# Performance work log

Measured on AMD Instinct MI355X. Metric: run time of the kernel, lower is better.

## Reference

```python
import jax, jax.numpy as jnp
import numpy as np

B, T = 256, 50
N_ITEMS = 100000
EMB = 256      # embedding
KBD = 128      # KBembedding == MN_dims
HID = 256      # layers[0] == layers[-1]
OUT = 256      # out_dim
NF = 10        # MN_nfactors == n_r


def setup_inputs() -> dict:
    key = jax.random.key(0)
    ks = jax.random.split(key, 18)
    s = 0.05
    return {
        "X": jax.random.randint(ks[0], (B, T), 0, N_ITEMS),
        "E": jax.random.normal(ks[1], (N_ITEMS, EMB), jnp.float32) * s,
        "KBE": jax.random.normal(ks[2], (N_ITEMS, KBD), jnp.float32) * s,
        "r_matrix": jax.random.normal(ks[3], (NF, KBD), jnp.float32) * s,
        "W_ih": jax.random.normal(ks[4], (3 * HID, EMB), jnp.float32) * s,
        "W_hh": jax.random.normal(ks[5], (3 * HID, HID), jnp.float32) * s,
        "b_ih": jnp.zeros((3 * HID,), jnp.float32),
        "b_hh": jnp.zeros((3 * HID,), jnp.float32),
        "MNu_W": jax.random.normal(ks[6], (KBD, HID), jnp.float32) * s,
        "MNu_b": jnp.zeros((KBD,), jnp.float32),
        "MNu2_W": jax.random.normal(ks[7], (HID, KBD + HID), jnp.float32) * s,
        "MNu2_b": jnp.zeros((HID,), jnp.float32),
        "MNea_W": jax.random.normal(ks[8], (KBD, KBD), jnp.float32) * s,
        "MNea_b": jnp.zeros((KBD,), jnp.float32),
        "mlp1_W": jax.random.normal(ks[9], (OUT, HID), jnp.float32) * s,
        "mlp1_b": jnp.zeros((OUT,), jnp.float32),
        "mlp2_W": jax.random.normal(ks[10], (OUT, EMB + KBD), jnp.float32) * s,
        "mlp2_b": jnp.zeros((OUT,), jnp.float32),
    }


def _gru_cell(x, h, W_ih, W_hh, b_ih, b_hh):
    # PyTorch GRUCell: gates stacked [r, z, n] along dim 0 of weights
    gi = x @ W_ih.T + b_ih
    gh = h @ W_hh.T + b_hh
    ir, iz, inn = jnp.split(gi, 3, axis=-1)
    hr, hz, hn = jnp.split(gh, 3, axis=-1)
    r = jax.nn.sigmoid(ir + hr)
    z = jax.nn.sigmoid(iz + hz)
    n = jnp.tanh(inn + r * hn)
    return (1.0 - z) * n + z * h


def reference(X, E, KBE, r_matrix, W_ih, W_hh, b_ih, b_hh,
              MNu_W, MNu_b, MNu2_W, MNu2_b, MNea_W, MNea_b,
              mlp1_W, mlp1_b, mlp2_W, mlp2_b):
    Bv, Tv = X.shape
    Em = E.at[0].set(0.0)     # mask row 0 of E
    KBm = KBE.at[0].set(0.0)  # mask row 0 of KBE
    Sx = Em[X]                # (B, T, EMB)
    KBItem = KBm[X]           # (B, T, KBD)

    def step(carry, xs):
        h, MN, y_sum = carry
        x_t, kb_t = xs                      # (B, EMB), (B, KBD)
        h = _gru_cell(x_t, h, W_ih, W_hh, b_ih, b_hh)
        y = h                                # dropout p=0 -> identity
        # gated memory write
        EA = jnp.tanh(kb_t @ MNea_W.T + MNea_b)          # (B, KBD)
        EA = EA[:, None, :] + r_matrix                    # (B, NF, KBD)
        gate = jax.nn.sigmoid(jnp.sum(MN * EA, axis=-1, keepdims=True))  # (B, NF, 1)
        MN = MN * (1.0 - gate) + EA * gate
        # attention read
        U = jnp.tanh(y @ MNu_W.T + MNu_b)                 # (B, KBD)
        AW = jax.nn.softmax(U @ r_matrix.T, axis=1)       # (B, NF)
        AC = jnp.einsum('bfd,bf->bd', MN, AW)             # (B, KBD)
        Ut = jnp.tanh(jnp.concatenate([y, AC], axis=-1) @ MNu2_W.T + MNu2_b)  # (B, HID)
        y_out = jnp.tanh(Ut @ mlp1_W.T + mlp1_b)          # (B, OUT)
        return (h, MN, y_sum + y_out), None

    init = (jnp.zeros((Bv, HID), Sx.dtype),
            jnp.zeros((Bv, NF, KBD), Sx.dtype),
            jnp.zeros((Bv, OUT), Sx.dtype))
    xs = (jnp.swapaxes(Sx, 0, 1), jnp.swapaxes(KBItem, 0, 1))  # (T, B, *)
    (h, MN, y_sum), _ = jax.lax.scan(step, init, xs)
    y = y_sum / Tv

    MergeE = jnp.concatenate([E, KBE], axis=1).at[0].set(0.0)  # (N, EMB+KBD)
    Sy = jnp.tanh(MergeE @ mlp2_W.T + mlp2_b)                  # (N, OUT)
    scores = jax.nn.log_softmax(y @ Sy.T, axis=1)              # (B, N)
    return scores, y
```

## Files before the change

kernel.cpp:

```cpp
#include <hip/hip_runtime.h>

typedef _Float16 f16;
typedef _Float16 f16x2 __attribute__((ext_vector_type(2)));
typedef _Float16 f16x8 __attribute__((ext_vector_type(8)));
typedef float f32x4 __attribute__((ext_vector_type(4)));
typedef int i32x4 __attribute__((ext_vector_type(4)));

#define MFMA16(a,b,c) __builtin_amdgcn_mfma_f32_16x16x32_f16(a,b,c,0,0,0)

#define NITEMS 100000
#define NBLK4  1563

#define OFF_WIH   0u
#define OFF_WHH   393216u
#define OFF_MNU   786432u
#define OFF_MNU2  851968u
#define OFF_MNEA  1048576u
#define OFF_MLP1  1081344u
#define OFF_MLP2  1212416u
#define OFF_WHHD  1409024u
#define OFF_GI    1802240u
#define OFF_TV    21463040u
#define OFF_MN    24739840u
#define OFF_YALL  57507840u
#define OFF_SY    64061440u
#define OFF_Y16   115261440u
#define OFF_PMAX  115392512u
#define OFF_PSUM  117030912u
#define OFF_LSE   118669312u

__device__ __forceinline__ float sigm(float x) { return 1.f / (1.f + __expf(-x)); }
__device__ __forceinline__ float tanh_fast(float x) {
  return 1.f - 2.f / (1.f + __expf(2.f * x));
}
__device__ __forceinline__ float fdot2(f16x2 a, f16x2 b, float c) {
#if defined(__has_builtin)
#if __has_builtin(__builtin_amdgcn_fdot2)
  return __builtin_amdgcn_fdot2(a, b, c, false);
#else
  return fmaf((float)a[1], (float)b[1], fmaf((float)a[0], (float)b[0], c));
#endif
#else
  return fmaf((float)a[1], (float)b[1], fmaf((float)a[0], (float)b[0], c));
#endif
}

__global__ __launch_bounds__(256) void k_pack(
    const float* s0, const float* s1, const float* s2, const float* s3,
    const float* s4, const float* s5, const float* s6, f16* base)
{
  int fid = blockIdx.x * 256 + threadIdx.x;
  if (fid >= 88064) {
    int g = fid - 88064;
    const float* sp = s1 + (size_t)g * 8;
    f16* dst = (f16*)((char*)base + OFF_WHHD);
    f16x8 v;
    #pragma unroll
    for (int j = 0; j < 8; j++) v[j] = (f16)sp[j];
    *(f16x8*)(dst + (size_t)g * 8) = v;
    return;
  }
  const float* src; f16* dst; int K, f;
  if (fid < 24576)      { src = s0; dst = base;          K = 256; f = fid; }
  else if (fid < 49152) { src = s1; dst = base + 196608; K = 256; f = fid - 24576; }
  else if (fid < 53248) { src = s2; dst = base + 393216; K = 256; f = fid - 49152; }
  else if (fid < 65536) { src = s3; dst = base + 425984; K = 384; f = fid - 53248; }
  else if (fid < 67584) { src = s4; dst = base + 524288; K = 128; f = fid - 65536; }
  else if (fid < 75776) { src = s5; dst = base + 540672; K = 256; f = fid - 67584; }
  else                  { src = s6; dst = base + 606208; K = 384; f = fid - 75776; }
  int lane = f & 63, t2 = f >> 6, KS = K >> 5;
  int ks = t2 % KS, nt = t2 / KS;
  int row = nt * 16 + (lane & 15), col = ks * 32 + ((lane >> 4) << 3);
  const float* sp = src + (size_t)row * K + col;
  f16x8 v;
  #pragma unroll
  for (int j = 0; j < 8; j++) v[j] = (f16)sp[j];
  *(f16x8*)(dst + (size_t)f * 8) = v;
}

__global__ __launch_bounds__(512) void k_prep(
    const int* __restrict__ X, const float* __restrict__ E,
    const f16* __restrict__ Wih_p, const float* __restrict__ bih,
    const float* __restrict__ bhh, f16* __restrict__ gi,
    const float* __restrict__ KBE, const f16* __restrict__ Wea_p,
    const float* __restrict__ bea, f16* __restrict__ tv)
{
  __shared__ __align__(16) char smem[66048];
  f16 (*At)[264] = (f16(*)[264])smem;
  f16* Lg2 = (f16*)(smem + 16896);
  int tid = threadIdx.x;
  int w = tid >> 6, lane = tid & 63, lr = lane & 15, lg = lane >> 4;
  if (blockIdx.x < 400) {
    int r0g = blockIdx.x * 32;
    int t = r0g >> 8;
    {
      int r = tid >> 4, c = (tid & 15) * 16;
      int b = (r0g + r) & 255;
      int item = X[b * 50 + t];
      if (item == 0) {
        #pragma unroll
        for (int j = 0; j < 16; j++) At[r][c + j] = (f16)0.f;
      } else {
        const float4* sp = (const float4*)(E + (size_t)item * 256 + c);
        #pragma unroll
        for (int q = 0; q < 4; q++) {
          float4 v = sp[q];
          At[r][c + q*4 + 0] = (f16)v.x; At[r][c + q*4 + 1] = (f16)v.y;
          At[r][c + q*4 + 2] = (f16)v.z; At[r][c + q*4 + 3] = (f16)v.w;
        }
      }
    }
    __syncthreads();
    f32x4 acc[2][6] = {};
    for (int ks = 0; ks < 8; ks++) {
      f16x8 a0 = *(const f16x8*)(&At[lr][ks * 32 + lg * 8]);
      f16x8 a1 = *(const f16x8*)(&At[16 + lr][ks * 32 + lg * 8]);
      #pragma unroll
      for (int j = 0; j < 6; j++) {
        int nt = w * 6 + j;
        f16x8 bf = *(const f16x8*)(Wih_p + ((size_t)((nt * 8 + ks) * 64 + lane) << 3));
        acc[0][j] = MFMA16(a0, bf, acc[0][j]);
        acc[1][j] = MFMA16(a1, bf, acc[1][j]);
      }
    }
    #pragma unroll
    for (int j = 0; j < 6; j++) {
      int col = (w * 6 + j) * 16 + lr;
      float bias = bih[col] + (col < 512 ? bhh[col] : 0.f);
      #pragma unroll
      for (int mt = 0; mt < 2; mt++)
        #pragma unroll
        for (int rr = 0; rr < 4; rr++)
          Lg2[(mt * 16 + lg * 4 + rr) * 768 + col] = (f16)(acc[mt][j][rr] + bias);
    }
    __syncthreads();
    f16* dst = gi + (size_t)r0g * 768;
    #pragma unroll
    for (int q = 0; q < 6; q++) {
      int u = q * 512 + tid;
      *(f16x8*)(dst + u * 8) = *(const f16x8*)(Lg2 + u * 8);
    }
  } else {
    int r0 = (blockIdx.x - 400) * 32;
    int t = r0 >> 8;
    {
      int r = tid >> 4, c = (tid & 15) * 8;
      int b = (r0 + r) & 255;
      int item = X[b * 50 + t];
      if (item == 0) {
        #pragma unroll
        for (int j = 0; j < 8; j++) At[r][c + j] = (f16)0.f;
      } else {
        const float4* sp = (const float4*)(KBE + (size_t)item * 128 + c);
        #pragma unroll
        for (int q = 0; q < 2; q++) {
          float4 v = sp[q];
          At[r][c + q*4 + 0] = (f16)v.x; At[r][c + q*4 + 1] = (f16)v.y;
          At[r][c + q*4 + 2] = (f16)v.z; At[r][c + q*4 + 3] = (f16)v.w;
        }
      }
    }
    __syncthreads();
    f32x4 acc[2] = {};
    for (int ks = 0; ks < 4; ks++) {
      f16x8 a0 = *(const f16x8*)(&At[lr][ks * 32 + lg * 8]);
      f16x8 a1 = *(const f16x8*)(&At[16 + lr][ks * 32 + lg * 8]);
      f16x8 bf = *(const f16x8*)(Wea_p + ((size_t)((w * 4 + ks) * 64 + lane) << 3));
      acc[0] = MFMA16(a0, bf, acc[0]);
      acc[1] = MFMA16(a1, bf, acc[1]);
    }
    f16* tvs = Lg2;
    int col = w * 16 + lr;
    float bias = bea[col];
    #pragma unroll
    for (int mt = 0; mt < 2; mt++)
      #pragma unroll
      for (int rr = 0; rr < 4; rr++)
        tvs[(mt * 16 + lg * 4 + rr) * 128 + col] = (f16)tanh_fast(acc[mt][rr] + bias);
    __syncthreads();
    {
      int row = tid >> 4, c = (tid & 15) * 8;
      *(f16x8*)(tv + (size_t)(r0 + row) * 128 + c) = *(const f16x8*)(tvs + row * 128 + c);
    }
  }
}

__global__ __launch_bounds__(1024) void k_fused2(
    const f16* __restrict__ Whh_d, const float* __restrict__ bhh,
    const f16* __restrict__ gi, f16* __restrict__ y_all,
    const f16* __restrict__ tv, const float* __restrict__ Rm, f16* __restrict__ MN,
    const float* __restrict__ E, const float* __restrict__ KBE,
    const f16* __restrict__ mlp2_p, const float* __restrict__ mlp2b, f16* __restrict__ Sy)
{
  __shared__ __align__(16) char smem[25088];
  int tid = threadIdx.x, w = tid >> 6, l = tid & 63;
  if (blockIdx.x < 256) {
    f16* hbuf = (f16*)smem;
    float* ghbuf = (float*)(smem + 1024);
    int b = blockIdx.x;
    int chunk = l >> 4, cl = l & 15;
    i32x4 Wv[3][8];
    #pragma unroll
    for (int j = 0; j < 3; j++) {
      int col = w * 48 + j * 16 + cl;
      const f16* wp = Whh_d + (size_t)col * 256 + chunk * 64;
      #pragma unroll
      for (int m = 0; m < 8; m++)
        Wv[j][m] = *(const i32x4*)(wp + m * 8);
    }
    float hprev = 0.f, bN = 0.f;
    f16 gr = (f16)0.f, gz = (f16)0.f, gn = (f16)0.f;
    if (tid < 256) {
      hbuf[(tid >> 6) * 72 + (tid & 63)] = (f16)0.f;
      bN = bhh[512 + tid];
      const f16* g0 = gi + (size_t)b * 768 + tid;
      gr = g0[0]; gz = g0[256]; gn = g0[512];
    }
    __syncthreads();
    const f16* hb = hbuf + chunk * 72;
    for (int t = 0; t < 50; t++) {
      float s0 = 0.f, s1 = 0.f, s2 = 0.f;
      #pragma unroll
      for (int m = 0; m < 8; m++) {
        i32x4 hw = *(const i32x4*)(hb + m * 8);
        #pragma unroll
        for (int p = 0; p < 4; p++) {
          f16x2 hp = __builtin_bit_cast(f16x2, hw[p]);
          s0 = fdot2(hp, __builtin_bit_cast(f16x2, Wv[0][m][p]), s0);
          s1 = fdot2(hp, __builtin_bit_cast(f16x2, Wv[1][m][p]), s1);
          s2 = fdot2(hp, __builtin_bit_cast(f16x2, Wv[2][m][p]), s2);
        }
      }
      s0 += __shfl_xor(s0, 16); s0 += __shfl_xor(s0, 32);
      s1 += __shfl_xor(s1, 16); s1 += __shfl_xor(s1, 32);
      s2 += __shfl_xor(s2, 16); s2 += __shfl_xor(s2, 32);
      if (l < 16) {
        ghbuf[w * 48 + l]      = s0;
        ghbuf[w * 48 + 16 + l] = s1;
        ghbuf[w * 48 + 32 + l] = s2;
      }
      __syncthreads();
      if (tid < 256) {
        int c = tid;
        float rg = sigm((float)gr + ghbuf[c]);
        float zg = sigm((float)gz + ghbuf[256 + c]);
        float ng = tanh_fast((float)gn + rg * (ghbuf[512 + c] + bN));
        float hv = ng + zg * (hprev - ng);
        hprev = hv;
        hbuf[(c >> 6) * 72 + (c & 63)] = (f16)hv;
        y_all[((size_t)t * 256 + b) * 256 + c] = (f16)hv;
        if (t < 49) {
          const f16* gN = gi + ((size_t)(t + 1) * 256 + b) * 768 + c;
          gr = gN[0]; gz = gN[256]; gn = gN[512];
        }
      }
      __syncthreads();
    }
  } else if (blockIdx.x < 416) {
    int lane = l;
    int pair = (blockIdx.x - 256) * 16 + w;
    int b = pair / 10, f = pair - (pair / 10) * 10;
    float r0_ = Rm[f * 128 + lane], r1_ = Rm[f * 128 + 64 + lane];
    float mn0 = 0.f, mn1 = 0.f;
    float c0 = (float)tv[(size_t)b * 128 + lane];
    float c1 = (float)tv[(size_t)b * 128 + 64 + lane];
    for (int t = 0; t < 50; t++) {
      float ea0 = c0 + r0_;
      float ea1 = c1 + r1_;
      if (t < 49) {
        size_t nb = ((size_t)(t + 1) * 256 + b) * 128;
        c0 = (float)tv[nb + lane];
        c1 = (float)tv[nb + 64 + lane];
      }
      float p = mn0 * ea0 + mn1 * ea1;
      #pragma unroll
      for (int off = 32; off > 0; off >>= 1) p += __shfl_xor(p, off);
      float g = sigm(p);
      mn0 += (ea0 - mn0) * g;
      mn1 += (ea1 - mn1) * g;
      size_t mb = (((size_t)t * 256 + b) * 10 + f) * 128;
      MN[mb + lane] = (f16)mn0;
      MN[mb + 64 + lane] = (f16)mn1;
    }
  } else {
    f16* At = (f16*)smem;
    int lane = l, lr = lane & 15, lg = lane >> 4;
    int i0 = (blockIdx.x - 416) * 32;
    {
      int r = tid >> 5;
      int item = i0 + r;
      int c = (tid & 31) * 8;
      if (item == 0) {
        #pragma unroll
        for (int j = 0; j < 8; j++) At[r * 392 + c + j] = (f16)0.f;
      } else {
        const float4* sp = (const float4*)(E + (size_t)item * 256 + c);
        #pragma unroll
        for (int q = 0; q < 2; q++) {
          float4 v = sp[q];
          At[r * 392 + c + q*4 + 0] = (f16)v.x; At[r * 392 + c + q*4 + 1] = (f16)v.y;
          At[r * 392 + c + q*4 + 2] = (f16)v.z; At[r * 392 + c + q*4 + 3] = (f16)v.w;
        }
      }
      int c2 = (tid & 31) * 4;
      if (item == 0) {
        #pragma unroll
        for (int j = 0; j < 4; j++) At[r * 392 + 256 + c2 + j] = (f16)0.f;
      } else {
        float4 v = *(const float4*)(KBE + (size_t)item * 128 + c2);
        At[r * 392 + 256 + c2 + 0] = (f16)v.x; At[r * 392 + 256 + c2 + 1] = (f16)v.y;
        At[r * 392 + 256 + c2 + 2] = (f16)v.z; At[r * 392 + 256 + c2 + 3] = (f16)v.w;
      }
    }
    __syncthreads();
    int mt = w & 1, ntp = w >> 1;
    f32x4 acc[2] = {};
    for (int ks = 0; ks < 12; ks++) {
      f16x8 a = *(const f16x8*)(&At[(mt * 16 + lr) * 392 + ks * 32 + lg * 8]);
      #pragma unroll
      for (int j = 0; j < 2; j++) {
        int nt = ntp * 2 + j;
        f16x8 bf = *(const f16x8*)(mlp2_p + ((size_t)((nt * 12 + ks) * 64 + lane) << 3));
        acc[j] = MFMA16(a, bf, acc[j]);
      }
    }
    #pragma unroll
    for (int j = 0; j < 2; j++) {
      int col = (ntp * 2 + j) * 16 + lr;
      float bias = mlp2b[col];
      #pragma unroll
      for (int rr = 0; rr < 4; rr++) {
        int item = i0 + mt * 16 + lg * 4 + rr;
        Sy[(size_t)item * 256 + col] = (f16)tanh_fast(acc[j][rr] + bias);
      }
    }
  }
}

__global__ __launch_bounds__(512) void k_uacut(
    const f16* __restrict__ y_all, const f16* __restrict__ MNu_p,
    const float* __restrict__ MNub, const float* __restrict__ Rm,
    const f16* __restrict__ MN,
    const f16* __restrict__ MNu2_p, const float* __restrict__ MNu2b,
    const f16* __restrict__ mlp1_p, const float* __restrict__ mlp1b,
    float* __restrict__ ypart)
{
  __shared__ __align__(16) char smem[25088];
  int tid = threadIdx.x, w = tid >> 6, lane = tid & 63, lr = lane & 15, lg = lane >> 4;
  f16   (*Aty)[264] = (f16(*)[264])smem;
  float (*Uf)[136]  = (float(*)[136])(smem + 8448);
  f16   (*Utl)[264] = (f16(*)[264])(smem + 8448);
  float (*Lg)[10]   = (float(*)[10])(smem + 17152);
  float (*Aw)[10]   = (float(*)[10])(smem + 17792);
  f16   (*ACs)[136] = (f16(*)[136])(smem + 18432);
  int r0 = blockIdx.x * 16;
  {
    int r = tid >> 5, c = (tid & 31) * 8;
    f16x8 v = *(const f16x8*)(y_all + (size_t)(r0 + r) * 256 + c);
    *(f16x8*)(&Aty[r][c]) = v;
  }
  __syncthreads();
  {
    f32x4 acc = {};
    for (int ks = 0; ks < 8; ks++) {
      f16x8 a = *(const f16x8*)(&Aty[lr][ks * 32 + lg * 8]);
      f16x8 bf = *(const f16x8*)(MNu_p + ((size_t)((w * 8 + ks) * 64 + lane) << 3));
      acc = MFMA16(a, bf, acc);
    }
    int col = w * 16 + lr;
    float bias = MNub[col];
    #pragma unroll
    for (int rr = 0; rr < 4; rr++)
      Uf[lg * 4 + rr][col] = tanh_fast(acc[rr] + bias);
  }
  __syncthreads();
  if (tid < 160) {
    int row = tid / 10, f = tid - (tid / 10) * 10;
    float s = 0.f;
    for (int d = 0; d < 128; d++) s += Uf[row][d] * Rm[f * 128 + d];
    Lg[row][f] = s;
  }
  __syncthreads();
  if (tid < 16) {
    float m = -1e30f;
    #pragma unroll
    for (int f = 0; f < 10; f++) m = fmaxf(m, Lg[tid][f]);
    float e[10], s = 0.f;
    #pragma unroll
    for (int f = 0; f < 10; f++) { e[f] = __expf(Lg[tid][f] - m); s += e[f]; }
    float inv = 1.f / s;
    #pragma unroll
    for (int f = 0; f < 10; f++) Aw[tid][f] = e[f] * inv;
  }
  __syncthreads();
  if (tid < 256) {
    int row = tid >> 4, d0 = (tid & 15) * 8;
    float a[8] = {0,0,0,0,0,0,0,0};
    for (int f = 0; f < 10; f++) {
      float wgt = Aw[row][f];
      f16x8 mv = *(const f16x8*)(MN + (((size_t)(r0 + row)) * 10 + f) * 128 + d0);
      #pragma unroll
      for (int q = 0; q < 8; q++) a[q] += wgt * (float)mv[q];
    }
    f16x8 o;
    #pragma unroll
    for (int q = 0; q < 8; q++) o[q] = (f16)a[q];
    *(f16x8*)(&ACs[row][d0]) = o;
  }
  __syncthreads();
  {
    f32x4 acc[2] = {};
    for (int ks = 0; ks < 12; ks++) {
      f16x8 a = (ks < 8)
        ? *(const f16x8*)(&Aty[lr][ks * 32 + lg * 8])
        : *(const f16x8*)(&ACs[lr][(ks - 8) * 32 + lg * 8]);
      #pragma unroll
      for (int j = 0; j < 2; j++) {
        f16x8 bf = *(const f16x8*)(MNu2_p + ((size_t)(((w * 2 + j) * 12 + ks) * 64 + lane) << 3));
        acc[j] = MFMA16(a, bf, acc[j]);
      }
    }
    __syncthreads();
    #pragma unroll
    for (int j = 0; j < 2; j++) {
      int col = (w * 2 + j) * 16 + lr;
      float bias = MNu2b[col];
      #pragma unroll
      for (int rr = 0; rr < 4; rr++)
        Utl[lg * 4 + rr][col] = (f16)tanh_fast(acc[j][rr] + bias);
    }
  }
  __syncthreads();
  {
    f32x4 acc2[2] = {};
    for (int ks = 0; ks < 8; ks++) {
      f16x8 a = *(const f16x8*)(&Utl[lr][ks * 32 + lg * 8]);
      #pragma unroll
      for (int j = 0; j < 2; j++) {
        f16x8 bf = *(const f16x8*)(mlp1_p + ((size_t)(((w * 2 + j) * 8 + ks) * 64 + lane) << 3));
        acc2[j] = MFMA16(a, bf, acc2[j]);
      }
    }
    #pragma unroll
    for (int j = 0; j < 2; j++) {
      int col = (w * 2 + j) * 16 + lr;
      float bias = mlp1b[col];
      #pragma unroll
      for (int rr = 0; rr < 4; rr++) {
        int row = r0 + lg * 4 + rr;
        ypart[(size_t)row * 256 + col] = tanh_fast(acc2[j][rr] + bias);
      }
    }
  }
}

__global__ __launch_bounds__(256) void k_yfin(
    const float* __restrict__ ypart, float* __restrict__ outy, f16* __restrict__ y16)
{
  int b = blockIdx.x, c = threadIdx.x;
  float s = 0.f;
  for (int t = 0; t < 50; t++) s += ypart[((size_t)t * 256 + b) * 256 + c];
  float v = s * (1.0f / 50.0f);
  outy[b * 256 + c] = v;
  y16[b * 256 + c] = (f16)v;
}

__global__ __launch_bounds__(512) void k_score0(
    const f16* __restrict__ y16, const f16* __restrict__ Sy,
    float* __restrict__ pmax, float* __restrict__ psum)
{
  __shared__ float pm[512], ps[512];
  int tid = threadIdx.x, w = tid >> 6, lane = tid & 63, lr = lane & 15, lg = lane >> 4;
  int i0 = blockIdx.x * 64;
  int mtb = (w >> 1) * 4, ntb = (w & 1) * 2;
  f32x4 acc[4][2] = {};
  for (int ks = 0; ks < 8; ks++) {
    f16x8 a[4];
    #pragma unroll
    for (int i = 0; i < 4; i++)
      a[i] = *(const f16x8*)(y16 + ((size_t)((mtb + i) * 16 + lr)) * 256 + ks * 32 + lg * 8);
    #pragma unroll
    for (int j = 0; j < 2; j++) {
      int item = i0 + (ntb + j) * 16 + lr;
      int ic = item < NITEMS ? item : (NITEMS - 1);
      f16x8 bv = *(const f16x8*)(Sy + (size_t)ic * 256 + ks * 32 + lg * 8);
      #pragma unroll
      for (int i = 0; i < 4; i++) acc[i][j] = MFMA16(a[i], bv, acc[i][j]);
    }
  }
  {
    int item0 = i0 + ntb * 16 + lr, item1 = item0 + 16;
    bool v0 = item0 < NITEMS, v1 = item1 < NITEMS;
    #pragma unroll
    for (int i = 0; i < 4; i++)
      #pragma unroll
      for (int rr = 0; rr < 4; rr++) {
        float x0 = v0 ? acc[i][0][rr] : -1e30f;
        float x1 = v1 ? acc[i][1][rr] : -1e30f;
        float m = fmaxf(x0, x1);
        m = fmaxf(m, __shfl_xor(m, 1)); m = fmaxf(m, __shfl_xor(m, 2));
        m = fmaxf(m, __shfl_xor(m, 4)); m = fmaxf(m, __shfl_xor(m, 8));
        float s = (v0 ? __expf(x0 - m) : 0.f) + (v1 ? __expf(x1 - m) : 0.f);
        s += __shfl_xor(s, 1); s += __shfl_xor(s, 2);
        s += __shfl_xor(s, 4); s += __shfl_xor(s, 8);
        if (lr == 0) {
          int row = (mtb + i) * 16 + lg * 4 + rr;
          pm[(w & 1) * 256 + row] = m;
          ps[(w & 1) * 256 + row] = s;
        }
      }
  }
  __syncthreads();
  if (tid < 256) {
    float m0 = pm[tid], m1 = pm[256 + tid];
    float s0 = ps[tid], s1 = ps[256 + tid];
    float M = fmaxf(m0, m1);
    float S = s0 * __expf(m0 - M) + s1 * __expf(m1 - M);
    pmax[(size_t)tid * 1600 + blockIdx.x] = M;
    psum[(size_t)tid * 1600 + blockIdx.x] = S;
  }
}

__global__ __launch_bounds__(256) void k_lse(
    const float* __restrict__ pmax, const float* __restrict__ psum, float* __restrict__ lse)
{
  int b = blockIdx.x, tid = threadIdx.x;
  __shared__ float red[256];
  float m = -1e30f;
  for (int i = tid; i < NBLK4; i += 256) m = fmaxf(m, pmax[(size_t)b * 1600 + i]);
  red[tid] = m; __syncthreads();
  for (int s = 128; s > 0; s >>= 1) {
    if (tid < s) red[tid] = fmaxf(red[tid], red[tid + s]);
    __syncthreads();
  }
  float M = red[0]; __syncthreads();
  float s = 0.f;
  for (int i = tid; i < NBLK4; i += 256)
    s += psum[(size_t)b * 1600 + i] * __expf(pmax[(size_t)b * 1600 + i] - M);
  red[tid] = s; __syncthreads();
  for (int q = 128; q > 0; q >>= 1) {
    if (tid < q) red[tid] += red[tid + q];
    __syncthreads();
  }
  if (tid == 0) lse[b] = M + logf(red[0]);
}

__global__ __launch_bounds__(512) void k_scores1(
    const f16* __restrict__ y16, const f16* __restrict__ Sy,
    const float* __restrict__ lse, float* __restrict__ out)
{
  __shared__ float lse_s[256];
  int tid = threadIdx.x, w = tid >> 6, lane = tid & 63, lr = lane & 15, lg = lane >> 4;
  if (tid < 256) lse_s[tid] = lse[tid];
  int i0 = blockIdx.x * 64;
  int mtb = (w >> 1) * 4, ntb = (w & 1) * 2;
  f32x4 acc[4][2] = {};
  for (int ks = 0; ks < 8; ks++) {
    f16x8 a[4];
    #pragma unroll
    for (int i = 0; i < 4; i++)
      a[i] = *(const f16x8*)(y16 + ((size_t)((mtb + i) * 16 + lr)) * 256 + ks * 32 + lg * 8);
    #pragma unroll
    for (int j = 0; j < 2; j++) {
      int item = i0 + (ntb + j) * 16 + lr;
      int ic = item < NITEMS ? item : (NITEMS - 1);
      f16x8 bv = *(const f16x8*)(Sy + (size_t)ic * 256 + ks * 32 + lg * 8);
      #pragma unroll
      for (int i = 0; i < 4; i++) acc[i][j] = MFMA16(a[i], bv, acc[i][j]);
    }
  }
  __syncthreads();
  #pragma unroll
  for (int i = 0; i < 4; i++)
    #pragma unroll
    for (int j = 0; j < 2; j++) {
      int c = i0 + (ntb + j) * 16 + lr;
      if (c < NITEMS) {
        #pragma unroll
        for (int rr = 0; rr < 4; rr++) {
          int row = (mtb + i) * 16 + lg * 4 + rr;
          out[(size_t)row * NITEMS + c] = acc[i][j][rr] - lse_s[row];
        }
      }
    }
}

extern "C" void kernel_launch(void* const* d_in, const int* in_sizes, int n_in,
                              void* d_out, int out_size, void* d_ws, size_t ws_size,
                              hipStream_t stream) {
  (void)in_sizes; (void)n_in; (void)out_size; (void)ws_size;
  const int*   X     = (const int*)d_in[0];
  const float* E     = (const float*)d_in[1];
  const float* KBE   = (const float*)d_in[2];
  const float* Rm    = (const float*)d_in[3];
  const float* Wih   = (const float*)d_in[4];
  const float* Whh   = (const float*)d_in[5];
  const float* bih   = (const float*)d_in[6];
  const float* bhh   = (const float*)d_in[7];
  const float* MNuW  = (const float*)d_in[8];
  const float* MNub  = (const float*)d_in[9];
  const float* MNu2W = (const float*)d_in[10];
  const float* MNu2b = (const float*)d_in[11];
  const float* MNeaW = (const float*)d_in[12];
  const float* MNeab = (const float*)d_in[13];
  const float* mlp1W = (const float*)d_in[14];
  const float* mlp1b = (const float*)d_in[15];
  const float* mlp2W = (const float*)d_in[16];
  const float* mlp2b = (const float*)d_in[17];

  char* ws = (char*)d_ws;
  f16*   Wih_p  = (f16*)(ws + OFF_WIH);
  f16*   MNu_p  = (f16*)(ws + OFF_MNU);
  f16*   MNu2_p = (f16*)(ws + OFF_MNU2);
  f16*   Wea_p  = (f16*)(ws + OFF_MNEA);
  f16*   mlp1_p = (f16*)(ws + OFF_MLP1);
  f16*   mlp2_p = (f16*)(ws + OFF_MLP2);
  f16*   Whh_d  = (f16*)(ws + OFF_WHHD);
  f16*   gi     = (f16*)(ws + OFF_GI);
  f16*   tv     = (f16*)(ws + OFF_TV);
  f16*   MN     = (f16*)(ws + OFF_MN);
  f16*   y_all  = (f16*)(ws + OFF_YALL);
  f16*   Sy     = (f16*)(ws + OFF_SY);
  float* ypart  = (float*)(ws + OFF_GI);
  f16*   y16    = (f16*)(ws + OFF_Y16);
  float* pmax   = (float*)(ws + OFF_PMAX);
  float* psum   = (float*)(ws + OFF_PSUM);
  float* lse    = (float*)(ws + OFF_LSE);
  float* outf   = (float*)d_out;

  k_pack<<<440, 256, 0, stream>>>(Wih, Whh, MNuW, MNu2W, MNeaW, mlp1W, mlp2W, (f16*)ws);
  k_prep<<<800, 512, 0, stream>>>(X, E, Wih_p, bih, bhh, gi, KBE, Wea_p, MNeab, tv);
  k_fused2<<<3541, 1024, 0, stream>>>(Whh_d, bhh, gi, y_all, tv, Rm, MN,
                                      E, KBE, mlp2_p, mlp2b, Sy);
  k_uacut<<<800, 512, 0, stream>>>(y_all, MNu_p, MNub, Rm, MN,
                                   MNu2_p, MNu2b, mlp1_p, mlp1b, ypart);
  k_yfin<<<256, 256, 0, stream>>>(ypart, outf + 25600000, y16);
  k_score0<<<NBLK4, 512, 0, stream>>>(y16, Sy, pmax, psum);
  k_lse<<<256, 256, 0, stream>>>(pmax, psum, lse);
  k_scores1<<<NBLK4, 512, 0, stream>>>(y16, Sy, lse, outf);
}
```

Before: 391.0 us.

## Process four batch rows per GRU recurrence block to reuse register-held W_hh

The GRU recurrence blocks now each handle four batch rows instead of one, so the W_hh slice held in registers serves four hidden vectors per step and all 1024 threads do the gate update. This cuts the number of recurrence blocks from 256 to 64 and the total grid accordingly, reducing redundant weight loads and idle threads. In exchange each step runs four times the dot-product work, plus more shuffles and register pressure, on fewer CUs, which may lengthen the serial critical path of the 50-step recurrence.

```diff
diff --git a/kernel.cpp b/kernel.cpp
--- a/kernel.cpp
+++ b/kernel.cpp
@@ -185,7 +185,7 @@
   }
 }
 
-__global__ __launch_bounds__(1024) void k_fused2(
+__global__ __launch_bounds__(1024) void k_fused3(
     const f16* __restrict__ Whh_d, const float* __restrict__ bhh,
     const f16* __restrict__ gi, f16* __restrict__ y_all,
     const f16* __restrict__ tv, const float* __restrict__ Rm, f16* __restrict__ MN,
@@ -194,10 +194,10 @@
 {
   __shared__ __align__(16) char smem[25088];
   int tid = threadIdx.x, w = tid >> 6, l = tid & 63;
-  if (blockIdx.x < 256) {
+  if (blockIdx.x < 64) {
     f16* hbuf = (f16*)smem;
-    float* ghbuf = (float*)(smem + 1024);
-    int b = blockIdx.x;
+    float* ghbuf = (float*)(smem + 2560);
+    int b0 = blockIdx.x * 4;
     int chunk = l >> 4, cl = l & 15;
     i32x4 Wv[3][8];
     #pragma unroll
@@ -208,57 +208,67 @@
       for (int m = 0; m < 8; m++)
         Wv[j][m] = *(const i32x4*)(wp + m * 8);
     }
-    float hprev = 0.f, bN = 0.f;
-    f16 gr = (f16)0.f, gz = (f16)0.f, gn = (f16)0.f;
-    if (tid < 256) {
-      hbuf[(tid >> 6) * 72 + (tid & 63)] = (f16)0.f;
-      bN = bhh[512 + tid];
-      const f16* g0 = gi + (size_t)b * 768 + tid;
-      gr = g0[0]; gz = g0[256]; gn = g0[512];
-    }
-    __syncthreads();
-    const f16* hb = hbuf + chunk * 72;
+    int q = tid >> 8, c = tid & 255;
+    int b = b0 + q;
+    float hprev = 0.f;
+    float bN = bhh[512 + c];
+    const f16* gB = gi + (size_t)b * 768 + c;
+    f16 gr = gB[0], gz = gB[256], gn = gB[512];
+    {
+      if (tid < 1024) ((f16*)hbuf)[tid] = (f16)0.f;
+      if (tid < 128)  ((f16*)hbuf)[1024 + tid] = (f16)0.f;
+    }
+    __syncthreads();
     for (int t = 0; t < 50; t++) {
-      float s0 = 0.f, s1 = 0.f, s2 = 0.f;
+      float s[4][3] = {};
       #pragma unroll
       for (int m = 0; m < 8; m++) {
-        i32x4 hw = *(const i32x4*)(hb + m * 8);
-        #pragma unroll
-        for (int p = 0; p < 4; p++) {
-          f16x2 hp = __builtin_bit_cast(f16x2, hw[p]);
-          s0 = fdot2(hp, __builtin_bit_cast(f16x2, Wv[0][m][p]), s0);
-          s1 = fdot2(hp, __builtin_bit_cast(f16x2, Wv[1][m][p]), s1);
-          s2 = fdot2(hp, __builtin_bit_cast(f16x2, Wv[2][m][p]), s2);
-        }
-      }
-      s0 += __shfl_xor(s0, 16); s0 += __shfl_xor(s0, 32);
-      s1 += __shfl_xor(s1, 16); s1 += __shfl_xor(s1, 32);
-      s2 += __shfl_xor(s2, 16); s2 += __shfl_xor(s2, 32);
+        #pragma unroll
+        for (int qq = 0; qq < 4; qq++) {
+          i32x4 hw = *(const i32x4*)(hbuf + qq * 288 + chunk * 72 + m * 8);
+          #pragma unroll
+          for (int p = 0; p < 4; p++) {
+            f16x2 hp = __builtin_bit_cast(f16x2, hw[p]);
+            s[qq][0] = fdot2(hp, __builtin_bit_cast(f16x2, Wv[0][m][p]), s[qq][0]);
+            s[qq][1] = fdot2(hp, __builtin_bit_cast(f16x2, Wv[1][m][p]), s[qq][1]);
+            s[qq][2] = fdot2(hp, __builtin_bit_cast(f16x2, Wv[2][m][p]), s[qq][2]);
+          }
+        }
+      }
+      #pragma unroll
+      for (int qq = 0; qq < 4; qq++)
+        #pragma unroll
+        for (int j = 0; j < 3; j++) {
+          s[qq][j] += __shfl_xor(s[qq][j], 16);
+          s[qq][j] += __shfl_xor(s[qq][j], 32);
+        }
       if (l < 16) {
-        ghbuf[w * 48 + l]      = s0;
-        ghbuf[w * 48 + 16 + l] = s1;
-        ghbuf[w * 48 + 32 + l] = s2;
+        #pragma unroll
+        for (int qq = 0; qq < 4; qq++) {
+          ghbuf[qq * 768 + w * 48 + l]      = s[qq][0];
+          ghbuf[qq * 768 + w * 48 + 16 + l] = s[qq][1];
+          ghbuf[qq * 768 + w * 48 + 32 + l] = s[qq][2];
+        }
       }
       __syncthreads();
-      if (tid < 256) {
-        int c = tid;
-        float rg = sigm((float)gr + ghbuf[c]);
-        float zg = sigm((float)gz + ghbuf[256 + c]);
-        float ng = tanh_fast((float)gn + rg * (ghbuf[512 + c] + bN));
+      {
+        float rg = sigm((float)gr + ghbuf[q * 768 + c]);
+        float zg = sigm((float)gz + ghbuf[q * 768 + 256 + c]);
+        float ng = tanh_fast((float)gn + rg * (ghbuf[q * 768 + 512 + c] + bN));
         float hv = ng + zg * (hprev - ng);
         hprev = hv;
-        hbuf[(c >> 6) * 72 + (c & 63)] = (f16)hv;
+        hbuf[q * 288 + (c >> 6) * 72 + (c & 63)] = (f16)hv;
         y_all[((size_t)t * 256 + b) * 256 + c] = (f16)hv;
         if (t < 49) {
-          const f16* gN = gi + ((size_t)(t + 1) * 256 + b) * 768 + c;
+          const f16* gN = gB + (size_t)(t + 1) * 196608;
           gr = gN[0]; gz = gN[256]; gn = gN[512];
         }
       }
       __syncthreads();
     }
-  } else if (blockIdx.x < 416) {
+  } else if (blockIdx.x < 224) {
     int lane = l;
-    int pair = (blockIdx.x - 256) * 16 + w;
+    int pair = (blockIdx.x - 64) * 16 + w;
     int b = pair / 10, f = pair - (pair / 10) * 10;
     float r0_ = Rm[f * 128 + lane], r1_ = Rm[f * 128 + 64 + lane];
     float mn0 = 0.f, mn1 = 0.f;
@@ -285,7 +295,7 @@
   } else {
     f16* At = (f16*)smem;
     int lane = l, lr = lane & 15, lg = lane >> 4;
-    int i0 = (blockIdx.x - 416) * 32;
+    int i0 = (blockIdx.x - 224) * 32;
     {
       int r = tid >> 5;
       int item = i0 + r;
@@ -296,10 +306,10 @@
       } else {
         const float4* sp = (const float4*)(E + (size_t)item * 256 + c);
         #pragma unroll
-        for (int q = 0; q < 2; q++) {
-          float4 v = sp[q];
-          At[r * 392 + c + q*4 + 0] = (f16)v.x; At[r * 392 + c + q*4 + 1] = (f16)v.y;
-          At[r * 392 + c + q*4 + 2] = (f16)v.z; At[r * 392 + c + q*4 + 3] = (f16)v.w;
+        for (int qq = 0; qq < 2; qq++) {
+          float4 v = sp[qq];
+          At[r * 392 + c + qq*4 + 0] = (f16)v.x; At[r * 392 + c + qq*4 + 1] = (f16)v.y;
+          At[r * 392 + c + qq*4 + 2] = (f16)v.z; At[r * 392 + c + qq*4 + 3] = (f16)v.w;
         }
       }
       int c2 = (tid & 31) * 4;
@@ -400,11 +410,11 @@
       float wgt = Aw[row][f];
       f16x8 mv = *(const f16x8*)(MN + (((size_t)(r0 + row)) * 10 + f) * 128 + d0);
       #pragma unroll
-      for (int q = 0; q < 8; q++) a[q] += wgt * (float)mv[q];
+      for (int qq = 0; qq < 8; qq++) a[qq] += wgt * (float)mv[qq];
     }
     f16x8 o;
     #pragma unroll
-    for (int q = 0; q < 8; q++) o[q] = (f16)a[q];
+    for (int qq = 0; qq < 8; qq++) o[qq] = (f16)a[qq];
     *(f16x8*)(&ACs[row][d0]) = o;
   }
   __syncthreads();
@@ -630,7 +640,7 @@
 
   k_pack<<<440, 256, 0, stream>>>(Wih, Whh, MNuW, MNu2W, MNeaW, mlp1W, mlp2W, (f16*)ws);
   k_prep<<<800, 512, 0, stream>>>(X, E, Wih_p, bih, bhh, gi, KBE, Wea_p, MNeab, tv);
-  k_fused2<<<3541, 1024, 0, stream>>>(Whh_d, bhh, gi, y_all, tv, Rm, MN,
+  k_fused3<<<3349, 1024, 0, stream>>>(Whh_d, bhh, gi, y_all, tv, Rm, MN,
                                       E, KBE, mlp2_p, mlp2b, Sy);
   k_uacut<<<800, 512, 0, stream>>>(y_all, MNu_p, MNub, Rm, MN,
                                    MNu2_p, MNu2b, mlp1_p, mlp1b, ypart);
```

New measurement: 457.5 us. 1.17x slower.
